# Kernel optimization log

Hardware: AMD Instinct MI355X
Metric: run time of the kernel (lower is better)

The kernel has to match this reference:

```python
import jax, jax.numpy as jnp
import numpy as np

BN, BE, B = 50000, 800000, 16
NE, EE, GE, EH, NH = 32, 32, 32, 128, 128  # emb dims, hidden dims


def clean(x):
    return jnp.nan_to_num(x, nan=0.0, posinf=0.0, neginf=0.0)


def _lin(key, fan_in, fan_out):
    k1, k2 = jax.random.split(key)
    s = 1.0 / np.sqrt(fan_in)
    return (jax.random.uniform(k1, (fan_in, fan_out), jnp.float32, -s, s),
            jax.random.uniform(k2, (fan_out,), jnp.float32, -s, s))


def setup_inputs() -> dict:
    key = jax.random.key(0)
    ks = jax.random.split(key, 20)
    inp = {
        "x": jax.random.normal(ks[0], (BN, 2), jnp.float32),
        "edge_index": jax.random.randint(ks[1], (2, BE), 0, BN, jnp.int32),
        "batch": jax.random.randint(ks[2], (BN,), 0, B, jnp.int32),
        "node_attr": jnp.ones((BN, 2), jnp.float32),
        "edge_attr": jax.random.uniform(ks[3], (BE, 2), jnp.float32) + 0.5,  # positive spacings
        "glob_attr": jax.random.uniform(ks[4], (B, 2), jnp.float32),
    }
    # encoders (output 2*emb each, 'Duplicated')
    inp["enc_node_W"], inp["enc_node_b"] = _lin(ks[5], 2, 2 * NE)
    inp["enc_edge_W"], inp["enc_edge_b"] = _lin(ks[6], 2, 2 * EE)
    inp["enc_glob_W"], inp["enc_glob_b"] = _lin(ks[7], 2, 2 * GE)
    inp["enc2_W"], inp["enc2_b"] = _lin(ks[8], 2, 2 * EE)
    # derivative MLP: 4*NE+2*EE -> EH -> 2*EE
    inp["dW1"], inp["db1"] = _lin(ks[9], 4 * NE + 2 * EE, EH)
    inp["dW2"], inp["db2"] = _lin(ks[10], EH, 2 * EE)
    # half-jacobian MLP: 4*EE -> EH -> 2*EE
    inp["hW1"], inp["hb1"] = _lin(ks[11], 4 * EE, EH)
    inp["hW2"], inp["hb2"] = _lin(ks[12], EH, 2 * EE)
    # jacobian MLP: 6*EE -> NH -> 2*NE
    inp["jW1"], inp["jb1"] = _lin(ks[13], 6 * EE, NH)
    inp["jW2"], inp["jb2"] = _lin(ks[14], NH, 2 * NE)
    # hessian MLP: 4*EE+2*EE -> NH -> 2*NE
    inp["sW1"], inp["sb1"] = _lin(ks[15], 6 * EE, NH)
    inp["sW2"], inp["sb2"] = _lin(ks[16], NH, 2 * NE)
    # node MLP: 6*NE+2*GE -> NH -> 2*NE
    inp["nW1"], inp["nb1"] = _lin(ks[17], 6 * NE + 2 * GE, NH)
    inp["nW2"], inp["nb2"] = _lin(ks[18], NH, 2 * NE)
    # decoder: 2*NE -> 2
    inp["decW"], inp["decb"] = _lin(ks[19], 2 * NE, 2)
    return inp


def reference(x, edge_index, batch, node_attr, edge_attr, glob_attr,
              enc_node_W, enc_node_b, enc_edge_W, enc_edge_b, enc_glob_W, enc_glob_b,
              enc2_W, enc2_b,
              dW1, db1, dW2, db2,
              hW1, hb1, hW2, hb2,
              jW1, jb1, jW2, jb2,
              sW1, sb1, sW2, sb2,
              nW1, nb1, nW2, nb2,
              decW, decb):
    relu = jax.nn.relu
    seg = lambda d, idx: jax.ops.segment_sum(d, idx, num_segments=BN)
    mlp = lambda t, W1, b1, W2, b2: relu(t @ W1 + b1) @ W2 + b2

    row, col = edge_index[0], edge_index[1]
    spacing = edge_attr                                 # [BE,2]
    inv_spacing = clean(1.0 / spacing)
    inv_double = clean(1.0 / (seg(spacing, row) + seg(spacing, col)))  # [BN,2]

    node_emb = relu(x @ enc_node_W + enc_node_b)        # [BN,2*NE]
    spacing_emb = relu(spacing @ enc_edge_W + enc_edge_b)  # [BE,2*EE]
    glob_emb = relu(glob_attr @ enc_glob_W + enc_glob_b)   # [B,2*GE]
    inv_spacing_emb = relu(inv_spacing @ enc2_W + enc2_b)  # [BE,2*EE]
    inv_double_emb = relu(inv_double @ enc2_W + enc2_b)    # [BN,2*EE]

    d_edge = mlp(jnp.concatenate([node_emb[row], node_emb[col], inv_spacing_emb], -1),
                 dW1, db1, dW2, db2)                    # [BE,2*EE]
    hj_plus = seg(d_edge, row)                          # [BN,2*EE]
    hj_minus = seg(d_edge, col)

    jac1 = seg(mlp(jnp.concatenate([spacing_emb, hj_plus[col]], -1), hW1, hb1, hW2, hb2), col)
    jac2 = seg(mlp(jnp.concatenate([spacing_emb, hj_minus[row]], -1), hW1, hb1, hW2, hb2), row)
    jac = mlp(jnp.concatenate([jac1, jac2, inv_double_emb], -1), jW1, jb1, jW2, jb2)  # [BN,2*NE]

    hess = mlp(jnp.concatenate([hj_plus, hj_minus, inv_double_emb], -1), sW1, sb1, sW2, sb2)

    res = mlp(jnp.concatenate([node_emb, jac, glob_emb[batch], hess], -1), nW1, nb1, nW2, nb2)
    return node_attr * (res @ decW + decb)              # [BN,2]
```

## Files before the change

kernel.cpp:

```cpp
#include <hip/hip_runtime.h>
#include <math.h>

#define BN 50000
#define BE 800000

__device__ __forceinline__ float relu_f(float v) { return fmaxf(v, 0.0f); }
__device__ __forceinline__ float inv_clean(float s) {
    float q = 1.0f / s;
    return isfinite(q) ? q : 0.0f;
}
__device__ __forceinline__ float inv_clean_fast(float s) {
    float q = __builtin_amdgcn_rcpf(s);
    return isfinite(q) ? q : 0.0f;
}

__global__ __launch_bounds__(256) void k_node_enc(
    const float* __restrict__ x, const float* __restrict__ W,
    const float* __restrict__ b, float* __restrict__ node_emb)
{
    int t = blockIdx.x * 256 + threadIdx.x;
    int i = t >> 6, l = t & 63;
    float v = fmaf(x[i*2], W[l], fmaf(x[i*2+1], W[64+l], b[l]));
    node_emb[t] = relu_f(v);
}


__global__ __launch_bounds__(256, 2) void k_uv(
    const float* __restrict__ ne, const float* __restrict__ dW1,
    float* __restrict__ u, float* __restrict__ v)
{
    extern __shared__ float lds[];
    float4* wpk = (float4*)lds;
    float*  xbase = lds + 16384;

    for (int idx = threadIdx.x; idx < 64*64; idx += 256) {
        int j = idx >> 6, l = idx & 63;
        float4 w;
        if (l < 32) w = ((const float4*)(dW1 + j*128))[l];
        else        w = ((const float4*)(dW1 + (64+j)*128))[l-32];
        wpk[idx] = w;
    }
    __syncthreads();

    const int wid = threadIdx.x >> 6, l = threadIdx.x & 63;
    float* xb = xbase + wid * 512;
    float4* xb4 = (float4*)xb;
    const int gw = blockIdx.x * 4 + wid;
    const int nw = gridDim.x * 4;

    for (int g = gw; g < BN/8; g += nw) {
        const int n0 = g * 8;
        const int q = l >> 5;
        #pragma unroll
        for (int r = 0; r < 2; r++) {
            int j = (l & 31) + 32*r;
            float v0 = ne[(n0 + q*4 + 0)*64 + j];
            float v1 = ne[(n0 + q*4 + 1)*64 + j];
            float v2 = ne[(n0 + q*4 + 2)*64 + j];
            float v3 = ne[(n0 + q*4 + 3)*64 + j];
            xb4[j*2 + q] = make_float4(v0, v1, v2, v3);
        }
        float4 acc[8];
        #pragma unroll
        for (int e = 0; e < 8; e++) acc[e] = make_float4(0,0,0,0);
        #pragma unroll 8
        for (int j = 0; j < 64; j++) {
            float4 wq = wpk[j*64 + l];
            float4 xa = xb4[j*2 + 0];
            float4 xc = xb4[j*2 + 1];
            acc[0].x = fmaf(xa.x, wq.x, acc[0].x); acc[0].y = fmaf(xa.x, wq.y, acc[0].y);
            acc[0].z = fmaf(xa.x, wq.z, acc[0].z); acc[0].w = fmaf(xa.x, wq.w, acc[0].w);
            acc[1].x = fmaf(xa.y, wq.x, acc[1].x); acc[1].y = fmaf(xa.y, wq.y, acc[1].y);
            acc[1].z = fmaf(xa.y, wq.z, acc[1].z); acc[1].w = fmaf(xa.y, wq.w, acc[1].w);
            acc[2].x = fmaf(xa.z, wq.x, acc[2].x); acc[2].y = fmaf(xa.z, wq.y, acc[2].y);
            acc[2].z = fmaf(xa.z, wq.z, acc[2].z); acc[2].w = fmaf(xa.z, wq.w, acc[2].w);
            acc[3].x = fmaf(xa.w, wq.x, acc[3].x); acc[3].y = fmaf(xa.w, wq.y, acc[3].y);
            acc[3].z = fmaf(xa.w, wq.z, acc[3].z); acc[3].w = fmaf(xa.w, wq.w, acc[3].w);
            acc[4].x = fmaf(xc.x, wq.x, acc[4].x); acc[4].y = fmaf(xc.x, wq.y, acc[4].y);
            acc[4].z = fmaf(xc.x, wq.z, acc[4].z); acc[4].w = fmaf(xc.x, wq.w, acc[4].w);
            acc[5].x = fmaf(xc.y, wq.x, acc[5].x); acc[5].y = fmaf(xc.y, wq.y, acc[5].y);
            acc[5].z = fmaf(xc.y, wq.z, acc[5].z); acc[5].w = fmaf(xc.y, wq.w, acc[5].w);
            acc[6].x = fmaf(xc.z, wq.x, acc[6].x); acc[6].y = fmaf(xc.z, wq.y, acc[6].y);
            acc[6].z = fmaf(xc.z, wq.z, acc[6].z); acc[6].w = fmaf(xc.z, wq.w, acc[6].w);
            acc[7].x = fmaf(xc.w, wq.x, acc[7].x); acc[7].y = fmaf(xc.w, wq.y, acc[7].y);
            acc[7].z = fmaf(xc.w, wq.z, acc[7].z); acc[7].w = fmaf(xc.w, wq.w, acc[7].w);
        }
        float* dst = (l < 32) ? (u + 4*l) : (v + 4*(l-32));
        #pragma unroll
        for (int e = 0; e < 8; e++) {
            *(float4*)(dst + (size_t)(n0+e)*128) = acc[e];
        }
    }
}

__global__ __launch_bounds__(256, 2) void k_tptm(
    const float* __restrict__ hjp, const float* __restrict__ hjm,
    const float* __restrict__ hW1,
    float* __restrict__ tp, float* __restrict__ tm)
{
    extern __shared__ float lds[];
    float4* wpk = (float4*)lds;
    float*  xbase = lds + 8192;

    for (int idx = threadIdx.x; idx < 32*64; idx += 256) {
        int j2 = idx >> 6, l = idx & 63;
        float2 lo = ((const float2*)(hW1 + (64 + 2*j2)*128))[l];
        float2 hi = ((const float2*)(hW1 + (64 + 2*j2 + 1)*128))[l];
        wpk[idx] = make_float4(lo.x, lo.y, hi.x, hi.y);
    }
    __syncthreads();

    const int wid = threadIdx.x >> 6, l = threadIdx.x & 63;
    float* xb = xbase + wid * 512;
    float4* xb4 = (float4*)xb;
    const int gw = blockIdx.x * 4 + wid;
    const int nw = gridDim.x * 4;
    const int NG = BN/8;

    for (int vg = gw; vg < 2*NG; vg += nw) {
        const float* in  = (vg < NG) ? hjp : hjm;
        float*       out = (vg < NG) ? tp  : tm;
        const int n0 = ((vg < NG) ? vg : vg - NG) * 8;
        const int q = l >> 5;
        #pragma unroll
        for (int r = 0; r < 2; r++) {
            int j = (l & 31) + 32*r;
            float v0 = in[(n0 + q*4 + 0)*64 + j];
            float v1 = in[(n0 + q*4 + 1)*64 + j];
            float v2 = in[(n0 + q*4 + 2)*64 + j];
            float v3 = in[(n0 + q*4 + 3)*64 + j];
            xb4[j*2 + q] = make_float4(v0, v1, v2, v3);
        }
        float a0[8] = {0,0,0,0,0,0,0,0}, a1[8] = {0,0,0,0,0,0,0,0};
        #pragma unroll 8
        for (int j2 = 0; j2 < 32; j2++) {
            float4 wq = wpk[j2*64 + l];
            float4 xa = xb4[(2*j2)*2 + 0];
            float4 xbv = xb4[(2*j2)*2 + 1];
            float4 xc = xb4[(2*j2+1)*2 + 0];
            float4 xd = xb4[(2*j2+1)*2 + 1];
            a0[0] = fmaf(xa.x, wq.x, fmaf(xc.x, wq.z, a0[0]));
            a1[0] = fmaf(xa.x, wq.y, fmaf(xc.x, wq.w, a1[0]));
            a0[1] = fmaf(xa.y, wq.x, fmaf(xc.y, wq.z, a0[1]));
            a1[1] = fmaf(xa.y, wq.y, fmaf(xc.y, wq.w, a1[1]));
            a0[2] = fmaf(xa.z, wq.x, fmaf(xc.z, wq.z, a0[2]));
            a1[2] = fmaf(xa.z, wq.y, fmaf(xc.z, wq.w, a1[2]));
            a0[3] = fmaf(xa.w, wq.x, fmaf(xc.w, wq.z, a0[3]));
            a1[3] = fmaf(xa.w, wq.y, fmaf(xc.w, wq.w, a1[3]));
            a0[4] = fmaf(xbv.x, wq.x, fmaf(xd.x, wq.z, a0[4]));
            a1[4] = fmaf(xbv.x, wq.y, fmaf(xd.x, wq.w, a1[4]));
            a0[5] = fmaf(xbv.y, wq.x, fmaf(xd.y, wq.z, a0[5]));
            a1[5] = fmaf(xbv.y, wq.y, fmaf(xd.y, wq.w, a1[5]));
            a0[6] = fmaf(xbv.z, wq.x, fmaf(xd.z, wq.z, a0[6]));
            a1[6] = fmaf(xbv.z, wq.y, fmaf(xd.z, wq.w, a1[6]));
            a0[7] = fmaf(xbv.w, wq.x, fmaf(xd.w, wq.z, a0[7]));
            a1[7] = fmaf(xbv.w, wq.y, fmaf(xd.w, wq.w, a1[7]));
        }
        #pragma unroll
        for (int e = 0; e < 8; e++) {
            *(float2*)(out + (size_t)(n0+e)*128 + 2*l) = make_float2(a0[e], a1[e]);
        }
    }
}

__global__ __launch_bounds__(256, 2) void k_edge1f(
    const int* __restrict__ ei, const float* __restrict__ ea,
    const float* __restrict__ u, const float* __restrict__ v,
    const float* __restrict__ e2w, const float* __restrict__ e2b,
    const float* __restrict__ dW1, const float* __restrict__ db1,
    const float* __restrict__ dW2, const float* __restrict__ db2,
    float* __restrict__ sumsp, float* __restrict__ hjp, float* __restrict__ hjm)
{
    extern __shared__ float lds[];
    float4* w1pk = (float4*)lds;
    float4* w2pk = (float4*)(lds + 8192);
    float*  bufbase = lds + 16384;

    for (int idx = threadIdx.x; idx < 32*64; idx += 256) {
        int j2 = idx >> 6, ll = idx & 63;
        float2 lo = ((const float2*)(dW1 + (128 + 2*j2)*128))[ll];
        float2 hi = ((const float2*)(dW1 + (128 + 2*j2 + 1)*128))[ll];
        w1pk[idx] = make_float4(lo.x, lo.y, hi.x, hi.y);
    }
    for (int idx = threadIdx.x; idx < 32*64; idx += 256) {
        int k4 = idx >> 6, ll = idx & 63;
        w2pk[idx] = make_float4(dW2[(4*k4+0)*64+ll], dW2[(4*k4+1)*64+ll],
                                dW2[(4*k4+2)*64+ll], dW2[(4*k4+3)*64+ll]);
    }
    __syncthreads();

    const int wid = threadIdx.x >> 6, l = threadIdx.x & 63;
    float* buf = bufbase + wid * 1024;
    float4* buf4 = (float4*)buf;

    const int jA = l >> 1;
    const int eh = l & 1;
    const float ewA0 = e2w[jA],      ewB0 = e2w[64+jA],    eb0v = e2b[jA];
    const float ewA1 = e2w[jA+32],   ewB1 = e2w[96+jA],    eb1v = e2b[jA+32];
    const float b1a = db1[2*l], b1b = db1[2*l+1];
    const float b2r = db2[l];

    const int gw = blockIdx.x * 4 + wid;
    const int nw = gridDim.x * 4;

    for (int g = gw; g < BE/8; g += nw) {
        const int e0 = g * 8;
        int4 r01 = *(const int4*)(ei + e0);
        int4 r2  = *(const int4*)(ei + e0 + 4);
        int4 c01 = *(const int4*)(ei + BE + e0);
        int4 c2  = *(const int4*)(ei + BE + e0 + 4);
        float4 sv0 = ((const float4*)(ea + 2*e0))[0];
        float4 sv1 = ((const float4*)(ea + 2*e0))[1];
        float4 sv2 = ((const float4*)(ea + 2*e0))[2];
        float4 sv3 = ((const float4*)(ea + 2*e0))[3];

        if (l < 32) {
            int e = l >> 2, wch = l & 3;
            int4 rA = (e & 4) ? r2 : r01;
            int rx = (e & 2) ? ((e & 1) ? rA.w : rA.z) : ((e & 1) ? rA.y : rA.x);
            int4 cA = (e & 4) ? c2 : c01;
            int cx = (e & 2) ? ((e & 1) ? cA.w : cA.z) : ((e & 1) ? cA.y : cA.x);
            float4 sA = (e & 4) ? ((e & 2) ? sv3 : sv2) : ((e & 2) ? sv1 : sv0);
            float s0e = (e & 1) ? sA.z : sA.x;
            float s1e = (e & 1) ? sA.w : sA.y;
            int node = (wch < 2) ? rx : cx;
            int comp = wch & 1;
            float val = comp ? s1e : s0e;
            atomicAdd(&sumsp[node*2 + comp], val);
        }

        {
            float4 svA = eh ? sv2 : sv0;
            float4 svB = eh ? sv3 : sv1;
            float q00 = inv_clean_fast(svA.x), q10 = inv_clean_fast(svA.y);
            float q01 = inv_clean_fast(svA.z), q11 = inv_clean_fast(svA.w);
            float q02 = inv_clean_fast(svB.x), q12 = inv_clean_fast(svB.y);
            float q03 = inv_clean_fast(svB.z), q13 = inv_clean_fast(svB.w);
            float4 p0, p1;
            p0.x = relu_f(fmaf(q00, ewA0, fmaf(q10, ewB0, eb0v)));
            p0.y = relu_f(fmaf(q01, ewA0, fmaf(q11, ewB0, eb0v)));
            p0.z = relu_f(fmaf(q02, ewA0, fmaf(q12, ewB0, eb0v)));
            p0.w = relu_f(fmaf(q03, ewA0, fmaf(q13, ewB0, eb0v)));
            p1.x = relu_f(fmaf(q00, ewA1, fmaf(q10, ewB1, eb1v)));
            p1.y = relu_f(fmaf(q01, ewA1, fmaf(q11, ewB1, eb1v)));
            p1.z = relu_f(fmaf(q02, ewA1, fmaf(q12, ewB1, eb1v)));
            p1.w = relu_f(fmaf(q03, ewA1, fmaf(q13, ewB1, eb1v)));
            buf4[jA*2 + eh]      = p0;
            buf4[(jA+32)*2 + eh] = p1;
        }

        float t0[8], t1[8];
        {
            const int rr[8] = {r01.x, r01.y, r01.z, r01.w, r2.x, r2.y, r2.z, r2.w};
            const int cc[8] = {c01.x, c01.y, c01.z, c01.w, c2.x, c2.y, c2.z, c2.w};
            #pragma unroll
            for (int e = 0; e < 8; e++) {
                float2 uu = *(const float2*)(u + (size_t)rr[e]*128 + 2*l);
                float2 vv = *(const float2*)(v + (size_t)cc[e]*128 + 2*l);
                t0[e] = b1a + uu.x + vv.x;
                t1[e] = b1b + uu.y + vv.y;
            }
        }

        #pragma unroll 8
        for (int j2 = 0; j2 < 32; j2++) {
            float4 wq = w1pk[j2*64 + l];
            float4 xa = buf4[(2*j2)*2 + 0];
            float4 xbv = buf4[(2*j2)*2 + 1];
            float4 xc = buf4[(2*j2+1)*2 + 0];
            float4 xd = buf4[(2*j2+1)*2 + 1];
            t0[0] = fmaf(xa.x, wq.x, fmaf(xc.x, wq.z, t0[0]));
            t1[0] = fmaf(xa.x, wq.y, fmaf(xc.x, wq.w, t1[0]));
            t0[1] = fmaf(xa.y, wq.x, fmaf(xc.y, wq.z, t0[1]));
            t1[1] = fmaf(xa.y, wq.y, fmaf(xc.y, wq.w, t1[1]));
            t0[2] = fmaf(xa.z, wq.x, fmaf(xc.z, wq.z, t0[2]));
            t1[2] = fmaf(xa.z, wq.y, fmaf(xc.z, wq.w, t1[2]));
            t0[3] = fmaf(xa.w, wq.x, fmaf(xc.w, wq.z, t0[3]));
            t1[3] = fmaf(xa.w, wq.y, fmaf(xc.w, wq.w, t1[3]));
            t0[4] = fmaf(xbv.x, wq.x, fmaf(xd.x, wq.z, t0[4]));
            t1[4] = fmaf(xbv.x, wq.y, fmaf(xd.x, wq.w, t1[4]));
            t0[5] = fmaf(xbv.y, wq.x, fmaf(xd.y, wq.z, t0[5]));
            t1[5] = fmaf(xbv.y, wq.y, fmaf(xd.y, wq.w, t1[5]));
            t0[6] = fmaf(xbv.z, wq.x, fmaf(xd.z, wq.z, t0[6]));
            t1[6] = fmaf(xbv.z, wq.y, fmaf(xd.z, wq.w, t1[6]));
            t0[7] = fmaf(xbv.w, wq.x, fmaf(xd.w, wq.z, t0[7]));
            t1[7] = fmaf(xbv.w, wq.y, fmaf(xd.w, wq.w, t1[7]));
        }

        #pragma unroll
        for (int e = 0; e < 8; e++) {
            *(float2*)(buf + e*128 + 2*l) = make_float2(relu_f(t0[e]), relu_f(t1[e]));
        }
        float o[8] = {0,0,0,0,0,0,0,0};
        #pragma unroll 8
        for (int k4 = 0; k4 < 32; k4++) {
            float4 wq = w2pk[k4*64 + l];
            #pragma unroll
            for (int e = 0; e < 8; e++) {
                float4 hb = *(const float4*)(buf + e*128 + 4*k4);
                o[e] = fmaf(hb.x, wq.x, fmaf(hb.y, wq.y,
                        fmaf(hb.z, wq.z, fmaf(hb.w, wq.w, o[e]))));
            }
        }
        {
            const int rr[8] = {r01.x, r01.y, r01.z, r01.w, r2.x, r2.y, r2.z, r2.w};
            const int cc[8] = {c01.x, c01.y, c01.z, c01.w, c2.x, c2.y, c2.z, c2.w};
            #pragma unroll
            for (int e = 0; e < 8; e++) {
                float ov = o[e] + b2r;
                atomicAdd(&hjp[(size_t)rr[e]*64 + l], ov);
                atomicAdd(&hjm[(size_t)cc[e]*64 + l], ov);
            }
        }
    }
}

__global__ __launch_bounds__(256, 2) void k_edge2f(
    const int* __restrict__ ei, const float* __restrict__ ea,
    const float* __restrict__ tp, const float* __restrict__ tm,
    const float* __restrict__ eew, const float* __restrict__ eeb,
    const float* __restrict__ hW1, const float* __restrict__ hb1,
    const float* __restrict__ hW2, const float* __restrict__ hb2,
    float* __restrict__ jac1, float* __restrict__ jac2)
{
    extern __shared__ float lds[];
    float4* w1pk = (float4*)lds;
    float4* w2pk = (float4*)(lds + 8192);
    float*  bufbase = lds + 16384;

    for (int idx = threadIdx.x; idx < 32*64; idx += 256) {
        int j2 = idx >> 6, ll = idx & 63;
        float2 lo = ((const float2*)(hW1 + (2*j2)*128))[ll];
        float2 hi = ((const float2*)(hW1 + (2*j2 + 1)*128))[ll];
        w1pk[idx] = make_float4(lo.x, lo.y, hi.x, hi.y);
    }
    for (int idx = threadIdx.x; idx < 32*64; idx += 256) {
        int k4 = idx >> 6, ll = idx & 63;
        w2pk[idx] = make_float4(hW2[(4*k4+0)*64+ll], hW2[(4*k4+1)*64+ll],
                                hW2[(4*k4+2)*64+ll], hW2[(4*k4+3)*64+ll]);
    }
    __syncthreads();

    const int wid = threadIdx.x >> 6, l = threadIdx.x & 63;
    float* buf = bufbase + wid * 1024;
    float4* buf4 = (float4*)buf;

    const int jA = l >> 1;
    const int eh = l & 1;
    const float ewA0 = eew[jA],    ewB0 = eew[64+jA],  eb0v = eeb[jA];
    const float ewA1 = eew[jA+32], ewB1 = eew[96+jA],  eb1v = eeb[jA+32];
    const float b1a = hb1[2*l], b1b = hb1[2*l+1];
    const float b2r = hb2[l];

    const int gw = blockIdx.x * 4 + wid;
    const int nw = gridDim.x * 4;

    for (int g = gw; g < BE/8; g += nw) {
        const int e0 = g * 8;
        int4 r01 = *(const int4*)(ei + e0);
        int4 r2  = *(const int4*)(ei + e0 + 4);
        int4 c01 = *(const int4*)(ei + BE + e0);
        int4 c2  = *(const int4*)(ei + BE + e0 + 4);
        float4 sv0 = ((const float4*)(ea + 2*e0))[0];
        float4 sv1 = ((const float4*)(ea + 2*e0))[1];
        float4 sv2 = ((const float4*)(ea + 2*e0))[2];
        float4 sv3 = ((const float4*)(ea + 2*e0))[3];

        {
            float4 svA = eh ? sv2 : sv0;
            float4 svB = eh ? sv3 : sv1;
            float4 p0, p1;
            p0.x = relu_f(fmaf(svA.x, ewA0, fmaf(svA.y, ewB0, eb0v)));
            p0.y = relu_f(fmaf(svA.z, ewA0, fmaf(svA.w, ewB0, eb0v)));
            p0.z = relu_f(fmaf(svB.x, ewA0, fmaf(svB.y, ewB0, eb0v)));
            p0.w = relu_f(fmaf(svB.z, ewA0, fmaf(svB.w, ewB0, eb0v)));
            p1.x = relu_f(fmaf(svA.x, ewA1, fmaf(svA.y, ewB1, eb1v)));
            p1.y = relu_f(fmaf(svA.z, ewA1, fmaf(svA.w, ewB1, eb1v)));
            p1.z = relu_f(fmaf(svB.x, ewA1, fmaf(svB.y, ewB1, eb1v)));
            p1.w = relu_f(fmaf(svB.z, ewA1, fmaf(svB.w, ewB1, eb1v)));
            buf4[jA*2 + eh]      = p0;
            buf4[(jA+32)*2 + eh] = p1;
        }

        const int rr[8] = {r01.x, r01.y, r01.z, r01.w, r2.x, r2.y, r2.z, r2.w};
        const int cc[8] = {c01.x, c01.y, c01.z, c01.w, c2.x, c2.y, c2.z, c2.w};

        float2 tpv[8];
        #pragma unroll
        for (int e = 0; e < 8; e++)
            tpv[e] = *(const float2*)(tp + (size_t)cc[e]*128 + 2*l);

        float t0[8], t1[8];
        #pragma unroll
        for (int e = 0; e < 8; e++) { t0[e] = b1a; t1[e] = b1b; }

        #pragma unroll 8
        for (int j2 = 0; j2 < 32; j2++) {
            float4 wq = w1pk[j2*64 + l];
            float4 xa = buf4[(2*j2)*2 + 0];
            float4 xbv = buf4[(2*j2)*2 + 1];
            float4 xc = buf4[(2*j2+1)*2 + 0];
            float4 xd = buf4[(2*j2+1)*2 + 1];
            t0[0] = fmaf(xa.x, wq.x, fmaf(xc.x, wq.z, t0[0]));
            t1[0] = fmaf(xa.x, wq.y, fmaf(xc.x, wq.w, t1[0]));
            t0[1] = fmaf(xa.y, wq.x, fmaf(xc.y, wq.z, t0[1]));
            t1[1] = fmaf(xa.y, wq.y, fmaf(xc.y, wq.w, t1[1]));
            t0[2] = fmaf(xa.z, wq.x, fmaf(xc.z, wq.z, t0[2]));
            t1[2] = fmaf(xa.z, wq.y, fmaf(xc.z, wq.w, t1[2]));
            t0[3] = fmaf(xa.w, wq.x, fmaf(xc.w, wq.z, t0[3]));
            t1[3] = fmaf(xa.w, wq.y, fmaf(xc.w, wq.w, t1[3]));
            t0[4] = fmaf(xbv.x, wq.x, fmaf(xd.x, wq.z, t0[4]));
            t1[4] = fmaf(xbv.x, wq.y, fmaf(xd.x, wq.w, t1[4]));
            t0[5] = fmaf(xbv.y, wq.x, fmaf(xd.y, wq.z, t0[5]));
            t1[5] = fmaf(xbv.y, wq.y, fmaf(xd.y, wq.w, t1[5]));
            t0[6] = fmaf(xbv.z, wq.x, fmaf(xd.z, wq.z, t0[6]));
            t1[6] = fmaf(xbv.z, wq.y, fmaf(xd.z, wq.w, t1[6]));
            t0[7] = fmaf(xbv.w, wq.x, fmaf(xd.w, wq.z, t0[7]));
            t1[7] = fmaf(xbv.w, wq.y, fmaf(xd.w, wq.w, t1[7]));
        }

        #pragma unroll
        for (int e = 0; e < 8; e++) {
            *(float2*)(buf + e*128 + 2*l) =
                make_float2(relu_f(t0[e] + tpv[e].x), relu_f(t1[e] + tpv[e].y));
        }
        float2 tmv[8];
        #pragma unroll
        for (int e = 0; e < 8; e++)
            tmv[e] = *(const float2*)(tm + (size_t)rr[e]*128 + 2*l);

        float o1[8] = {0,0,0,0,0,0,0,0};
        #pragma unroll 8
        for (int k4 = 0; k4 < 32; k4++) {
            float4 wq = w2pk[k4*64 + l];
            #pragma unroll
            for (int e = 0; e < 8; e++) {
                float4 hb = *(const float4*)(buf + e*128 + 4*k4);
                o1[e] = fmaf(hb.x, wq.x, fmaf(hb.y, wq.y,
                         fmaf(hb.z, wq.z, fmaf(hb.w, wq.w, o1[e]))));
            }
        }
        #pragma unroll
        for (int e = 0; e < 8; e++)
            atomicAdd(&jac1[(size_t)cc[e]*64 + l], o1[e] + b2r);

        #pragma unroll
        for (int e = 0; e < 8; e++) {
            *(float2*)(buf + e*128 + 2*l) =
                make_float2(relu_f(t0[e] + tmv[e].x), relu_f(t1[e] + tmv[e].y));
        }
        float o2[8] = {0,0,0,0,0,0,0,0};
        #pragma unroll 8
        for (int k4 = 0; k4 < 32; k4++) {
            float4 wq = w2pk[k4*64 + l];
            #pragma unroll
            for (int e = 0; e < 8; e++) {
                float4 hb = *(const float4*)(buf + e*128 + 4*k4);
                o2[e] = fmaf(hb.x, wq.x, fmaf(hb.y, wq.y,
                         fmaf(hb.z, wq.z, fmaf(hb.w, wq.w, o2[e]))));
            }
        }
        #pragma unroll
        for (int e = 0; e < 8; e++)
            atomicAdd(&jac2[(size_t)rr[e]*64 + l], o2[e] + b2r);
    }
}

__global__ __launch_bounds__(256) void k_edge1(
    const int* __restrict__ ei, const float* __restrict__ ea,
    const float* __restrict__ node_emb,
    const float* __restrict__ e2w_g, const float* __restrict__ e2b_g,
    const float* __restrict__ dW1, const float* __restrict__ db1,
    const float* __restrict__ dW2, const float* __restrict__ db2,
    float* __restrict__ sumsp, float* __restrict__ hjp, float* __restrict__ hjm)
{
    extern __shared__ float lds[];
    float* w1 = lds;
    float* b1 = w1 + 192*128;
    float* w2 = b1 + 128;
    float* b2 = w2 + 128*64;
    float* ew = b2 + 64;
    float* eb = ew + 128;
    float* xreg = eb + 64;
    float* hreg = xreg + 4*768;

    for (int idx = threadIdx.x; idx < 192*128; idx += 256) w1[idx] = dW1[idx];
    for (int idx = threadIdx.x; idx < 128*64; idx += 256)  w2[idx] = dW2[idx];
    if (threadIdx.x < 128) { b1[threadIdx.x] = db1[threadIdx.x]; ew[threadIdx.x] = e2w_g[threadIdx.x]; }
    if (threadIdx.x < 64)  { b2[threadIdx.x] = db2[threadIdx.x]; eb[threadIdx.x] = e2b_g[threadIdx.x]; }
    __syncthreads();

    const int wid = threadIdx.x >> 6, l = threadIdx.x & 63;
    float* xbuf = xreg + wid * 768;
    float* hbuf = hreg + wid * 512;
    const int gw = blockIdx.x * 4 + wid;
    const int nw = gridDim.x * 4;

    for (int g = gw; g < BE/4; g += nw) {
        const int e0 = g * 4;
        int r[4], c[4];
        float s0[4], s1[4];
        #pragma unroll
        for (int e = 0; e < 4; e++) {
            r[e]  = ei[e0+e];
            c[e]  = ei[BE + e0+e];
            s0[e] = ea[(e0+e)*2+0];
            s1[e] = ea[(e0+e)*2+1];
        }
        if (l < 16) {
            int e = l >> 2, wch = l & 3;
            int node = (wch < 2) ? r[e] : c[e];
            float v = (wch & 1) ? s1[e] : s0[e];
            atomicAdd(&sumsp[node*2 + (wch & 1)], v);
        }
        float ar[4], cr[4], ir[4];
        #pragma unroll
        for (int e = 0; e < 4; e++) {
            ar[e] = node_emb[r[e]*64 + l];
            cr[e] = node_emb[c[e]*64 + l];
            float q0 = inv_clean(s0[e]), q1 = inv_clean(s1[e]);
            ir[e] = relu_f(fmaf(q0, ew[l], fmaf(q1, ew[64+l], eb[l])));
        }
        ((float4*)xbuf)[l]       = make_float4(ar[0], ar[1], ar[2], ar[3]);
        ((float4*)xbuf)[64 + l]  = make_float4(cr[0], cr[1], cr[2], cr[3]);
        ((float4*)xbuf)[128 + l] = make_float4(ir[0], ir[1], ir[2], ir[3]);

        float acc0[4] = {0,0,0,0}, acc1[4] = {0,0,0,0};
        #pragma unroll 8
        for (int j = 0; j < 192; j++) {
            float4 xv = ((const float4*)xbuf)[j];
            float2 wv = ((const float2*)(w1 + j*128))[l];
            acc0[0] = fmaf(xv.x, wv.x, acc0[0]);
            acc0[1] = fmaf(xv.y, wv.x, acc0[1]);
            acc0[2] = fmaf(xv.z, wv.x, acc0[2]);
            acc0[3] = fmaf(xv.w, wv.x, acc0[3]);
            acc1[0] = fmaf(xv.x, wv.y, acc1[0]);
            acc1[1] = fmaf(xv.y, wv.y, acc1[1]);
            acc1[2] = fmaf(xv.z, wv.y, acc1[2]);
            acc1[3] = fmaf(xv.w, wv.y, acc1[3]);
        }
        float bb0 = b1[2*l], bb1 = b1[2*l+1];
        #pragma unroll
        for (int e = 0; e < 4; e++) {
            float2 h = make_float2(relu_f(acc0[e]+bb0), relu_f(acc1[e]+bb1));
            ((float2*)(hbuf + e*128))[l] = h;
        }
        float o[4] = {0,0,0,0};
        #pragma unroll 8
        for (int k = 0; k < 128; k++) {
            float wv = w2[k*64 + l];
            o[0] = fmaf(hbuf[0*128+k], wv, o[0]);
            o[1] = fmaf(hbuf[1*128+k], wv, o[1]);
            o[2] = fmaf(hbuf[2*128+k], wv, o[2]);
            o[3] = fmaf(hbuf[3*128+k], wv, o[3]);
        }
        float bo = b2[l];
        #pragma unroll
        for (int e = 0; e < 4; e++) {
            float ov = o[e] + bo;
            atomicAdd(&hjp[r[e]*64 + l], ov);
            atomicAdd(&hjm[c[e]*64 + l], ov);
        }
    }
}

__global__ __launch_bounds__(256) void k_edge2(
    const int* __restrict__ ei, const float* __restrict__ ea,
    const float* __restrict__ hjp, const float* __restrict__ hjm,
    const float* __restrict__ eew_g, const float* __restrict__ eeb_g,
    const float* __restrict__ hW1, const float* __restrict__ hb1,
    const float* __restrict__ hW2, const float* __restrict__ hb2,
    float* __restrict__ jac1, float* __restrict__ jac2)
{
    extern __shared__ float lds[];
    float* w1 = lds;
    float* b1 = w1 + 128*128;
    float* w2 = b1 + 128;
    float* b2 = w2 + 128*64;
    float* ew = b2 + 64;
    float* eb = ew + 128;
    float* base = eb + 64;

    for (int idx = threadIdx.x; idx < 128*128; idx += 256) w1[idx] = hW1[idx];
    for (int idx = threadIdx.x; idx < 128*64; idx += 256)  w2[idx] = hW2[idx];
    if (threadIdx.x < 128) { b1[threadIdx.x] = hb1[threadIdx.x]; ew[threadIdx.x] = eew_g[threadIdx.x]; }
    if (threadIdx.x < 64)  { b2[threadIdx.x] = hb2[threadIdx.x]; eb[threadIdx.x] = eeb_g[threadIdx.x]; }
    __syncthreads();

    const int wid = threadIdx.x >> 6, l = threadIdx.x & 63;
    float* x1 = base + wid*2048;
    float* x2 = x1 + 512;
    float* h1 = x2 + 512;
    float* h2 = h1 + 512;
    const int gw = blockIdx.x * 4 + wid;
    const int nw = gridDim.x * 4;

    for (int g = gw; g < BE/4; g += nw) {
        const int e0 = g * 4;
        int r[4], c[4];
        float se[4], pa[4], pb[4];
        #pragma unroll
        for (int e = 0; e < 4; e++) {
            r[e] = ei[e0+e];
            c[e] = ei[BE + e0+e];
            float sp0 = ea[(e0+e)*2+0], sp1 = ea[(e0+e)*2+1];
            se[e] = relu_f(fmaf(sp0, ew[l], fmaf(sp1, ew[64+l], eb[l])));
            pa[e] = hjp[c[e]*64 + l];
            pb[e] = hjm[r[e]*64 + l];
        }
        ((float4*)x1)[l]      = make_float4(se[0], se[1], se[2], se[3]);
        ((float4*)x1)[64 + l] = make_float4(pa[0], pa[1], pa[2], pa[3]);
        ((float4*)x2)[l]      = make_float4(se[0], se[1], se[2], se[3]);
        ((float4*)x2)[64 + l] = make_float4(pb[0], pb[1], pb[2], pb[3]);

        float a0[4]={0,0,0,0}, a1[4]={0,0,0,0}, b0v[4]={0,0,0,0}, b1v[4]={0,0,0,0};
        #pragma unroll 8
        for (int j = 0; j < 128; j++) {
            float2 wv = ((const float2*)(w1 + j*128))[l];
            float4 xa = ((const float4*)x1)[j];
            float4 xb = ((const float4*)x2)[j];
            a0[0]=fmaf(xa.x,wv.x,a0[0]); a0[1]=fmaf(xa.y,wv.x,a0[1]);
            a0[2]=fmaf(xa.z,wv.x,a0[2]); a0[3]=fmaf(xa.w,wv.x,a0[3]);
            a1[0]=fmaf(xa.x,wv.y,a1[0]); a1[1]=fmaf(xa.y,wv.y,a1[1]);
            a1[2]=fmaf(xa.z,wv.y,a1[2]); a1[3]=fmaf(xa.w,wv.y,a1[3]);
            b0v[0]=fmaf(xb.x,wv.x,b0v[0]); b0v[1]=fmaf(xb.y,wv.x,b0v[1]);
            b0v[2]=fmaf(xb.z,wv.x,b0v[2]); b0v[3]=fmaf(xb.w,wv.x,b0v[3]);
            b1v[0]=fmaf(xb.x,wv.y,b1v[0]); b1v[1]=fmaf(xb.y,wv.y,b1v[1]);
            b1v[2]=fmaf(xb.z,wv.y,b1v[2]); b1v[3]=fmaf(xb.w,wv.y,b1v[3]);
        }
        float bb0 = b1[2*l], bb1 = b1[2*l+1];
        #pragma unroll
        for (int e = 0; e < 4; e++) {
            ((float2*)(h1 + e*128))[l] = make_float2(relu_f(a0[e]+bb0), relu_f(a1[e]+bb1));
            ((float2*)(h2 + e*128))[l] = make_float2(relu_f(b0v[e]+bb0), relu_f(b1v[e]+bb1));
        }
        float oA[4]={0,0,0,0}, oB[4]={0,0,0,0};
        #pragma unroll 8
        for (int k = 0; k < 128; k++) {
            float wv = w2[k*64 + l];
            oA[0]=fmaf(h1[0*128+k],wv,oA[0]); oA[1]=fmaf(h1[1*128+k],wv,oA[1]);
            oA[2]=fmaf(h1[2*128+k],wv,oA[2]); oA[3]=fmaf(h1[3*128+k],wv,oA[3]);
            oB[0]=fmaf(h2[0*128+k],wv,oB[0]); oB[1]=fmaf(h2[1*128+k],wv,oB[1]);
            oB[2]=fmaf(h2[2*128+k],wv,oB[2]); oB[3]=fmaf(h2[3*128+k],wv,oB[3]);
        }
        float bo = b2[l];
        #pragma unroll
        for (int e = 0; e < 4; e++) {
            atomicAdd(&jac1[c[e]*64 + l], oA[e] + bo);
            atomicAdd(&jac2[r[e]*64 + l], oB[e] + bo);
        }
    }
}

__global__ __launch_bounds__(256) void k_node_mlp(
    const float* __restrict__ A, const float* __restrict__ Bv,
    const float* __restrict__ sumsp,
    const float* __restrict__ e2w_g, const float* __restrict__ e2b_g,
    const float* __restrict__ W1g, const float* __restrict__ b1g,
    const float* __restrict__ W2g, const float* __restrict__ b2g,
    float* __restrict__ outp)
{
    extern __shared__ float lds[];
    float* w1 = lds;
    float* b1 = w1 + 192*128;
    float* w2 = b1 + 128;
    float* b2 = w2 + 128*64;
    float* ew = b2 + 64;
    float* eb = ew + 128;
    float* xreg = eb + 64;
    float* hreg = xreg + 4*768;

    for (int idx = threadIdx.x; idx < 192*128; idx += 256) w1[idx] = W1g[idx];
    for (int idx = threadIdx.x; idx < 128*64; idx += 256)  w2[idx] = W2g[idx];
    if (threadIdx.x < 128) { b1[threadIdx.x] = b1g[threadIdx.x]; ew[threadIdx.x] = e2w_g[threadIdx.x]; }
    if (threadIdx.x < 64)  { b2[threadIdx.x] = b2g[threadIdx.x]; eb[threadIdx.x] = e2b_g[threadIdx.x]; }
    __syncthreads();

    const int wid = threadIdx.x >> 6, l = threadIdx.x & 63;
    float* xbuf = xreg + wid * 768;
    float* hbuf = hreg + wid * 512;
    const int gw = blockIdx.x * 4 + wid;
    const int nw = gridDim.x * 4;

    for (int g = gw; g < BN/4; g += nw) {
        const int i0 = g * 4;
        float av[4], bv[4], iv[4];
        #pragma unroll
        for (int e = 0; e < 4; e++) {
            int i = i0 + e;
            av[e] = A[i*64 + l];
            bv[e] = Bv[i*64 + l];
            float q0 = inv_clean(sumsp[i*2+0]);
            float q1 = inv_clean(sumsp[i*2+1]);
            iv[e] = relu_f(fmaf(q0, ew[l], fmaf(q1, ew[64+l], eb[l])));
        }
        ((float4*)xbuf)[l]       = make_float4(av[0], av[1], av[2], av[3]);
        ((float4*)xbuf)[64 + l]  = make_float4(bv[0], bv[1], bv[2], bv[3]);
        ((float4*)xbuf)[128 + l] = make_float4(iv[0], iv[1], iv[2], iv[3]);

        float acc0[4] = {0,0,0,0}, acc1[4] = {0,0,0,0};
        #pragma unroll 8
        for (int j = 0; j < 192; j++) {
            float4 xv = ((const float4*)xbuf)[j];
            float2 wv = ((const float2*)(w1 + j*128))[l];
            acc0[0] = fmaf(xv.x, wv.x, acc0[0]);
            acc0[1] = fmaf(xv.y, wv.x, acc0[1]);
            acc0[2] = fmaf(xv.z, wv.x, acc0[2]);
            acc0[3] = fmaf(xv.w, wv.x, acc0[3]);
            acc1[0] = fmaf(xv.x, wv.y, acc1[0]);
            acc1[1] = fmaf(xv.y, wv.y, acc1[1]);
            acc1[2] = fmaf(xv.z, wv.y, acc1[2]);
            acc1[3] = fmaf(xv.w, wv.y, acc1[3]);
        }
        float bb0 = b1[2*l], bb1 = b1[2*l+1];
        #pragma unroll
        for (int e = 0; e < 4; e++) {
            ((float2*)(hbuf + e*128))[l] = make_float2(relu_f(acc0[e]+bb0), relu_f(acc1[e]+bb1));
        }
        float o[4] = {0,0,0,0};
        #pragma unroll 8
        for (int k = 0; k < 128; k++) {
            float wv = w2[k*64 + l];
            o[0] = fmaf(hbuf[0*128+k], wv, o[0]);
            o[1] = fmaf(hbuf[1*128+k], wv, o[1]);
            o[2] = fmaf(hbuf[2*128+k], wv, o[2]);
            o[3] = fmaf(hbuf[3*128+k], wv, o[3]);
        }
        float bo = b2[l];
        #pragma unroll
        for (int e = 0; e < 4; e++) outp[(i0+e)*64 + l] = o[e] + bo;
    }
}

__global__ __launch_bounds__(256) void k_node_final(
    const float* __restrict__ node_emb, const float* __restrict__ jacv,
    const float* __restrict__ hessv,
    const int* __restrict__ batch, const float* __restrict__ ga,
    const float* __restrict__ gw_g, const float* __restrict__ gb_g,
    const float* __restrict__ nW1, const float* __restrict__ nb1,
    const float* __restrict__ nW2, const float* __restrict__ nb2,
    const float* __restrict__ decW, const float* __restrict__ decb,
    const float* __restrict__ node_attr, float* __restrict__ outp)
{
    extern __shared__ float lds[];
    float* w1 = lds;
    float* b1 = w1 + 256*128;
    float* b2 = b1 + 128;
    float* gw = b2 + 64;
    float* gb = gw + 128;
    float* dw = gb + 64;
    float* db = dw + 128;
    float* xreg = db + 4;
    float* hreg = xreg + 4*1024;

    for (int idx = threadIdx.x; idx < 256*128; idx += 256) w1[idx] = nW1[idx];
    if (threadIdx.x < 128) { b1[threadIdx.x] = nb1[threadIdx.x]; gw[threadIdx.x] = gw_g[threadIdx.x]; dw[threadIdx.x] = decW[threadIdx.x]; }
    if (threadIdx.x < 64)  { b2[threadIdx.x] = nb2[threadIdx.x]; gb[threadIdx.x] = gb_g[threadIdx.x]; }
    if (threadIdx.x < 2)   { db[threadIdx.x] = decb[threadIdx.x]; }
    __syncthreads();

    const int wid = threadIdx.x >> 6, l = threadIdx.x & 63;
    float* xbuf = xreg + wid * 1024;
    float* hbuf = hreg + wid * 512;
    const int gwv = blockIdx.x * 4 + wid;
    const int nw = gridDim.x * 4;

    for (int g = gwv; g < BN/4; g += nw) {
        const int i0 = g * 4;
        float ne[4], jv[4], ge[4], hv[4];
        #pragma unroll
        for (int e = 0; e < 4; e++) {
            int i = i0 + e;
            ne[e] = node_emb[i*64 + l];
            jv[e] = jacv[i*64 + l];
            hv[e] = hessv[i*64 + l];
            int gi = batch[i];
            ge[e] = relu_f(fmaf(ga[gi*2], gw[l], fmaf(ga[gi*2+1], gw[64+l], gb[l])));
        }
        ((float4*)xbuf)[l]       = make_float4(ne[0], ne[1], ne[2], ne[3]);
        ((float4*)xbuf)[64 + l]  = make_float4(jv[0], jv[1], jv[2], jv[3]);
        ((float4*)xbuf)[128 + l] = make_float4(ge[0], ge[1], ge[2], ge[3]);
        ((float4*)xbuf)[192 + l] = make_float4(hv[0], hv[1], hv[2], hv[3]);

        float acc0[4] = {0,0,0,0}, acc1[4] = {0,0,0,0};
        #pragma unroll 8
        for (int j = 0; j < 256; j++) {
            float4 xv = ((const float4*)xbuf)[j];
            float2 wv = ((const float2*)(w1 + j*128))[l];
            acc0[0] = fmaf(xv.x, wv.x, acc0[0]);
            acc0[1] = fmaf(xv.y, wv.x, acc0[1]);
            acc0[2] = fmaf(xv.z, wv.x, acc0[2]);
            acc0[3] = fmaf(xv.w, wv.x, acc0[3]);
            acc1[0] = fmaf(xv.x, wv.y, acc1[0]);
            acc1[1] = fmaf(xv.y, wv.y, acc1[1]);
            acc1[2] = fmaf(xv.z, wv.y, acc1[2]);
            acc1[3] = fmaf(xv.w, wv.y, acc1[3]);
        }
        float bb0 = b1[2*l], bb1 = b1[2*l+1];
        #pragma unroll
        for (int e = 0; e < 4; e++) {
            ((float2*)(hbuf + e*128))[l] = make_float2(relu_f(acc0[e]+bb0), relu_f(acc1[e]+bb1));
        }
        float o[4] = {0,0,0,0};
        #pragma unroll 8
        for (int k = 0; k < 128; k++) {
            float wv = nW2[k*64 + l];
            o[0] = fmaf(hbuf[0*128+k], wv, o[0]);
            o[1] = fmaf(hbuf[1*128+k], wv, o[1]);
            o[2] = fmaf(hbuf[2*128+k], wv, o[2]);
            o[3] = fmaf(hbuf[3*128+k], wv, o[3]);
        }
        float bo = b2[l];
        #pragma unroll
        for (int e = 0; e < 4; e++) hbuf[e*128 + l] = o[e] + bo;

        int e2 = l >> 4, sub = l & 15, j2 = sub >> 3, part = sub & 7;
        float s = 0.0f;
        #pragma unroll
        for (int kk = 0; kk < 8; kk++) {
            int k = part*8 + kk;
            s = fmaf(hbuf[e2*128 + k], dw[k*2 + j2], s);
        }
        s += __shfl_xor(s, 1);
        s += __shfl_xor(s, 2);
        s += __shfl_xor(s, 4);
        if (part == 0) {
            int i = i0 + e2;
            outp[i*2 + j2] = (s + db[j2]) * node_attr[i*2 + j2];
        }
    }
}

extern "C" void kernel_launch(void* const* d_in, const int* in_sizes, int n_in,
                              void* d_out, int out_size, void* d_ws, size_t ws_size,
                              hipStream_t stream) {
    const float* x          = (const float*)d_in[0];
    const int*   ei         = (const int*)  d_in[1];
    const int*   batch      = (const int*)  d_in[2];
    const float* node_attr  = (const float*)d_in[3];
    const float* edge_attr  = (const float*)d_in[4];
    const float* glob_attr  = (const float*)d_in[5];
    const float* enc_node_W = (const float*)d_in[6];
    const float* enc_node_b = (const float*)d_in[7];
    const float* enc_edge_W = (const float*)d_in[8];
    const float* enc_edge_b = (const float*)d_in[9];
    const float* enc_glob_W = (const float*)d_in[10];
    const float* enc_glob_b = (const float*)d_in[11];
    const float* enc2_W     = (const float*)d_in[12];
    const float* enc2_b     = (const float*)d_in[13];
    const float* dW1 = (const float*)d_in[14]; const float* db1 = (const float*)d_in[15];
    const float* dW2 = (const float*)d_in[16]; const float* db2 = (const float*)d_in[17];
    const float* hW1 = (const float*)d_in[18]; const float* hb1 = (const float*)d_in[19];
    const float* hW2 = (const float*)d_in[20]; const float* hb2 = (const float*)d_in[21];
    const float* jW1 = (const float*)d_in[22]; const float* jb1 = (const float*)d_in[23];
    const float* jW2 = (const float*)d_in[24]; const float* jb2 = (const float*)d_in[25];
    const float* sW1 = (const float*)d_in[26]; const float* sb1 = (const float*)d_in[27];
    const float* sW2 = (const float*)d_in[28]; const float* sb2 = (const float*)d_in[29];
    const float* nW1 = (const float*)d_in[30]; const float* nb1 = (const float*)d_in[31];
    const float* nW2 = (const float*)d_in[32]; const float* nb2 = (const float*)d_in[33];
    const float* decW = (const float*)d_in[34]; const float* decb = (const float*)d_in[35];

    float* ws = (float*)d_ws;
    const size_t NEED_FAST = 28900000ull * sizeof(float);

    if (ws_size >= NEED_FAST) {
        float* ne    = ws;
        float* u     = ne + 3200000;
        float* v     = u + 6400000;
        float* hjp   = v + 6400000;
        float* hjm   = hjp + 3200000;
        float* jac1  = hjm + 3200000;
        float* jac2  = jac1 + 3200000;
        float* sumsp = jac2 + 3200000;

        hipMemsetAsync(hjp, 0, (size_t)4*3200000*sizeof(float), stream);
        hipMemsetAsync(sumsp, 0, (size_t)100000*sizeof(float), stream);

        k_node_enc<<<12500, 256, 0, stream>>>(x, enc_node_W, enc_node_b, ne);

        size_t lds_uv = 18432u * sizeof(float);
        k_uv<<<512, 256, lds_uv, stream>>>(ne, dW1, u, v);

        size_t lds_e = 20480u * sizeof(float);
        k_edge1f<<<512, 256, lds_e, stream>>>(ei, edge_attr, u, v, enc2_W, enc2_b,
                                              dW1, db1, dW2, db2, sumsp, hjp, hjm);

        size_t lds_tptm = 10240u * sizeof(float);
        k_tptm<<<512, 256, lds_tptm, stream>>>(hjp, hjm, hW1, u, v);

        k_edge2f<<<512, 256, lds_e, stream>>>(ei, edge_attr, u, v,
                                              enc_edge_W, enc_edge_b,
                                              hW1, hb1, hW2, hb2, jac1, jac2);

        size_t lds3 = 38272u * sizeof(float);
        k_node_mlp<<<256, 256, lds3, stream>>>(jac1, jac2, sumsp, enc2_W, enc2_b,
                                               jW1, jb1, jW2, jb2, jac1);
        k_node_mlp<<<256, 256, lds3, stream>>>(hjp, hjm, sumsp, enc2_W, enc2_b,
                                               sW1, sb1, sW2, sb2, hjp);

        size_t lds4 = 39428u * sizeof(float);
        k_node_final<<<256, 256, lds4, stream>>>(ne, jac1, hjp,
                                                 batch, glob_attr, enc_glob_W, enc_glob_b,
                                                 nW1, nb1, nW2, nb2, decW, decb,
                                                 node_attr, (float*)d_out);
    } else {
        float* node_emb = ws;
        float* hjp   = node_emb + 3200000;
        float* hjm   = hjp + 3200000;
        float* jac1  = hjm + 3200000;
        float* jac2  = jac1 + 3200000;
        float* sumsp = jac2 + 3200000;

        hipMemsetAsync(hjp, 0, (size_t)4*3200000*sizeof(float), stream);
        hipMemsetAsync(sumsp, 0, (size_t)100000*sizeof(float), stream);

        k_node_enc<<<12500, 256, 0, stream>>>(x, enc_node_W, enc_node_b, node_emb);

        size_t lds1 = 38272u * sizeof(float);
        k_edge1<<<256, 256, lds1, stream>>>(ei, edge_attr, node_emb, enc2_W, enc2_b,
                                            dW1, db1, dW2, db2, sumsp, hjp, hjm);

        size_t lds2 = 33152u * sizeof(float);
        k_edge2<<<256, 256, lds2, stream>>>(ei, edge_attr, hjp, hjm,
                                            enc_edge_W, enc_edge_b,
                                            hW1, hb1, hW2, hb2, jac1, jac2);

        size_t lds3 = 38272u * sizeof(float);
        k_node_mlp<<<256, 256, lds3, stream>>>(jac1, jac2, sumsp, enc2_W, enc2_b,
                                               jW1, jb1, jW2, jb2, jac1);
        k_node_mlp<<<256, 256, lds3, stream>>>(hjp, hjm, sumsp, enc2_W, enc2_b,
                                               sW1, sb1, sW2, sb2, hjp);

        size_t lds4 = 39428u * sizeof(float);
        k_node_final<<<256, 256, lds4, stream>>>(node_emb, jac1, hjp,
                                                 batch, glob_attr, enc_glob_W, enc_glob_b,
                                                 nW1, nb1, nW2, nb2, decW, decb,
                                                 node_attr, (float*)d_out);
    }
}
```

Measured before the change: 2.139 ms.

## Move MLP weights from LDS to pre-packed global memory to raise occupancy

Weight matrices that every block used to stage into LDS are now packed once into global scratch by small pack kernels, or read straight from global in the node kernels. The main kernels are served through the cache instead. With LDS use cut to per-wave activation buffers, launch bounds rise to 6 (4 for node kernels) and grids grow to 1536/1024 blocks to improve latency hiding. The trade-off is that weight loads now go through the L1/L2 cache rather than LDS. The packed weights are stored in the output buffer as scratch before the final kernel overwrites it.

```diff
diff --git a/kernel.cpp b/kernel.cpp
--- a/kernel.cpp
+++ b/kernel.cpp
@@ -14,6 +14,37 @@
     return isfinite(q) ? q : 0.0f;
 }
 
+__global__ __launch_bounds__(256) void k_pack_w1(
+    const float* __restrict__ W, int r0, float4* __restrict__ dst)
+{
+    int t = blockIdx.x * 256 + threadIdx.x;
+    if (t >= 2048) return;
+    int j2 = t >> 6, l = t & 63;
+    const float* ra = W + (size_t)(r0 + 2*j2) * 128 + 2*l;
+    const float* rb = W + (size_t)(r0 + 2*j2 + 1) * 128 + 2*l;
+    dst[t] = make_float4(ra[0], ra[1], rb[0], rb[1]);
+}
+__global__ __launch_bounds__(256) void k_pack_w2(
+    const float* __restrict__ W2, float4* __restrict__ dst)
+{
+    int t = blockIdx.x * 256 + threadIdx.x;
+    if (t >= 2048) return;
+    int k4 = t >> 6, l = t & 63;
+    dst[t] = make_float4(W2[(4*k4+0)*64+l], W2[(4*k4+1)*64+l],
+                         W2[(4*k4+2)*64+l], W2[(4*k4+3)*64+l]);
+}
+__global__ __launch_bounds__(256) void k_pack_uv(
+    const float* __restrict__ dW1, float4* __restrict__ dst)
+{
+    int t = blockIdx.x * 256 + threadIdx.x;
+    if (t >= 4096) return;
+    int j = t >> 6, l = t & 63;
+    float4 w;
+    if (l < 32) w = ((const float4*)(dW1 + (size_t)j*128))[l];
+    else        w = ((const float4*)(dW1 + (size_t)(64+j)*128))[l-32];
+    dst[t] = w;
+}
+
 __global__ __launch_bounds__(256) void k_node_enc(
     const float* __restrict__ x, const float* __restrict__ W,
     const float* __restrict__ b, float* __restrict__ node_emb)
@@ -25,26 +56,13 @@
 }
 
 
-__global__ __launch_bounds__(256, 2) void k_uv(
-    const float* __restrict__ ne, const float* __restrict__ dW1,
+__global__ __launch_bounds__(256, 6) void k_uv(
+    const float* __restrict__ ne, const float4* __restrict__ guv,
     float* __restrict__ u, float* __restrict__ v)
 {
     extern __shared__ float lds[];
-    float4* wpk = (float4*)lds;
-    float*  xbase = lds + 16384;
-
-    for (int idx = threadIdx.x; idx < 64*64; idx += 256) {
-        int j = idx >> 6, l = idx & 63;
-        float4 w;
-        if (l < 32) w = ((const float4*)(dW1 + j*128))[l];
-        else        w = ((const float4*)(dW1 + (64+j)*128))[l-32];
-        wpk[idx] = w;
-    }
-    __syncthreads();
-
     const int wid = threadIdx.x >> 6, l = threadIdx.x & 63;
-    float* xb = xbase + wid * 512;
-    float4* xb4 = (float4*)xb;
+    float4* xb4 = (float4*)(lds + wid * 512);
     const int gw = blockIdx.x * 4 + wid;
     const int nw = gridDim.x * 4;
 
@@ -65,7 +83,7 @@
         for (int e = 0; e < 8; e++) acc[e] = make_float4(0,0,0,0);
         #pragma unroll 8
         for (int j = 0; j < 64; j++) {
-            float4 wq = wpk[j*64 + l];
+            float4 wq = guv[j*64 + l];
             float4 xa = xb4[j*2 + 0];
             float4 xc = xb4[j*2 + 1];
             acc[0].x = fmaf(xa.x, wq.x, acc[0].x); acc[0].y = fmaf(xa.x, wq.y, acc[0].y);
@@ -93,26 +111,14 @@
     }
 }
 
-__global__ __launch_bounds__(256, 2) void k_tptm(
+__global__ __launch_bounds__(256, 6) void k_tptm(
     const float* __restrict__ hjp, const float* __restrict__ hjm,
-    const float* __restrict__ hW1,
+    const float4* __restrict__ gtp,
     float* __restrict__ tp, float* __restrict__ tm)
 {
     extern __shared__ float lds[];
-    float4* wpk = (float4*)lds;
-    float*  xbase = lds + 8192;
-
-    for (int idx = threadIdx.x; idx < 32*64; idx += 256) {
-        int j2 = idx >> 6, l = idx & 63;
-        float2 lo = ((const float2*)(hW1 + (64 + 2*j2)*128))[l];
-        float2 hi = ((const float2*)(hW1 + (64 + 2*j2 + 1)*128))[l];
-        wpk[idx] = make_float4(lo.x, lo.y, hi.x, hi.y);
-    }
-    __syncthreads();
-
     const int wid = threadIdx.x >> 6, l = threadIdx.x & 63;
-    float* xb = xbase + wid * 512;
-    float4* xb4 = (float4*)xb;
+    float4* xb4 = (float4*)(lds + wid * 512);
     const int gw = blockIdx.x * 4 + wid;
     const int nw = gridDim.x * 4;
     const int NG = BN/8;
@@ -134,7 +140,7 @@
         float a0[8] = {0,0,0,0,0,0,0,0}, a1[8] = {0,0,0,0,0,0,0,0};
         #pragma unroll 8
         for (int j2 = 0; j2 < 32; j2++) {
-            float4 wq = wpk[j2*64 + l];
+            float4 wq = gtp[j2*64 + l];
             float4 xa = xb4[(2*j2)*2 + 0];
             float4 xbv = xb4[(2*j2)*2 + 1];
             float4 xc = xb4[(2*j2+1)*2 + 0];
@@ -163,34 +169,17 @@
     }
 }
 
-__global__ __launch_bounds__(256, 2) void k_edge1f(
+__global__ __launch_bounds__(256, 6) void k_edge1f(
     const int* __restrict__ ei, const float* __restrict__ ea,
     const float* __restrict__ u, const float* __restrict__ v,
     const float* __restrict__ e2w, const float* __restrict__ e2b,
-    const float* __restrict__ dW1, const float* __restrict__ db1,
-    const float* __restrict__ dW2, const float* __restrict__ db2,
+    const float4* __restrict__ gw1, const float* __restrict__ db1,
+    const float4* __restrict__ gw2, const float* __restrict__ db2,
     float* __restrict__ sumsp, float* __restrict__ hjp, float* __restrict__ hjm)
 {
     extern __shared__ float lds[];
-    float4* w1pk = (float4*)lds;
-    float4* w2pk = (float4*)(lds + 8192);
-    float*  bufbase = lds + 16384;
-
-    for (int idx = threadIdx.x; idx < 32*64; idx += 256) {
-        int j2 = idx >> 6, ll = idx & 63;
-        float2 lo = ((const float2*)(dW1 + (128 + 2*j2)*128))[ll];
-        float2 hi = ((const float2*)(dW1 + (128 + 2*j2 + 1)*128))[ll];
-        w1pk[idx] = make_float4(lo.x, lo.y, hi.x, hi.y);
-    }
-    for (int idx = threadIdx.x; idx < 32*64; idx += 256) {
-        int k4 = idx >> 6, ll = idx & 63;
-        w2pk[idx] = make_float4(dW2[(4*k4+0)*64+ll], dW2[(4*k4+1)*64+ll],
-                                dW2[(4*k4+2)*64+ll], dW2[(4*k4+3)*64+ll]);
-    }
-    __syncthreads();
-
     const int wid = threadIdx.x >> 6, l = threadIdx.x & 63;
-    float* buf = bufbase + wid * 1024;
+    float* buf = lds + wid * 1024;
     float4* buf4 = (float4*)buf;
 
     const int jA = l >> 1;
@@ -264,7 +253,7 @@
 
         #pragma unroll 8
         for (int j2 = 0; j2 < 32; j2++) {
-            float4 wq = w1pk[j2*64 + l];
+            float4 wq = gw1[j2*64 + l];
             float4 xa = buf4[(2*j2)*2 + 0];
             float4 xbv = buf4[(2*j2)*2 + 1];
             float4 xc = buf4[(2*j2+1)*2 + 0];
@@ -294,7 +283,7 @@
         float o[8] = {0,0,0,0,0,0,0,0};
         #pragma unroll 8
         for (int k4 = 0; k4 < 32; k4++) {
-            float4 wq = w2pk[k4*64 + l];
+            float4 wq = gw2[k4*64 + l];
             #pragma unroll
             for (int e = 0; e < 8; e++) {
                 float4 hb = *(const float4*)(buf + e*128 + 4*k4);
@@ -315,34 +304,17 @@
     }
 }
 
-__global__ __launch_bounds__(256, 2) void k_edge2f(
+__global__ __launch_bounds__(256, 6) void k_edge2f(
     const int* __restrict__ ei, const float* __restrict__ ea,
     const float* __restrict__ tp, const float* __restrict__ tm,
     const float* __restrict__ eew, const float* __restrict__ eeb,
-    const float* __restrict__ hW1, const float* __restrict__ hb1,
-    const float* __restrict__ hW2, const float* __restrict__ hb2,
+    const float4* __restrict__ gw1, const float* __restrict__ hb1,
+    const float4* __restrict__ gw2, const float* __restrict__ hb2,
     float* __restrict__ jac1, float* __restrict__ jac2)
 {
     extern __shared__ float lds[];
-    float4* w1pk = (float4*)lds;
-    float4* w2pk = (float4*)(lds + 8192);
-    float*  bufbase = lds + 16384;
-
-    for (int idx = threadIdx.x; idx < 32*64; idx += 256) {
-        int j2 = idx >> 6, ll = idx & 63;
-        float2 lo = ((const float2*)(hW1 + (2*j2)*128))[ll];
-        float2 hi = ((const float2*)(hW1 + (2*j2 + 1)*128))[ll];
-        w1pk[idx] = make_float4(lo.x, lo.y, hi.x, hi.y);
-    }
-    for (int idx = threadIdx.x; idx < 32*64; idx += 256) {
-        int k4 = idx >> 6, ll = idx & 63;
-        w2pk[idx] = make_float4(hW2[(4*k4+0)*64+ll], hW2[(4*k4+1)*64+ll],
-                                hW2[(4*k4+2)*64+ll], hW2[(4*k4+3)*64+ll]);
-    }
-    __syncthreads();
-
     const int wid = threadIdx.x >> 6, l = threadIdx.x & 63;
-    float* buf = bufbase + wid * 1024;
+    float* buf = lds + wid * 1024;
     float4* buf4 = (float4*)buf;
 
     const int jA = l >> 1;
@@ -396,7 +368,7 @@
 
         #pragma unroll 8
         for (int j2 = 0; j2 < 32; j2++) {
-            float4 wq = w1pk[j2*64 + l];
+            float4 wq = gw1[j2*64 + l];
             float4 xa = buf4[(2*j2)*2 + 0];
             float4 xbv = buf4[(2*j2)*2 + 1];
             float4 xc = buf4[(2*j2+1)*2 + 0];
@@ -432,7 +404,7 @@
         float o1[8] = {0,0,0,0,0,0,0,0};
         #pragma unroll 8
         for (int k4 = 0; k4 < 32; k4++) {
-            float4 wq = w2pk[k4*64 + l];
+            float4 wq = gw2[k4*64 + l];
             #pragma unroll
             for (int e = 0; e < 8; e++) {
                 float4 hb = *(const float4*)(buf + e*128 + 4*k4);
@@ -452,7 +424,7 @@
         float o2[8] = {0,0,0,0,0,0,0,0};
         #pragma unroll 8
         for (int k4 = 0; k4 < 32; k4++) {
-            float4 wq = w2pk[k4*64 + l];
+            float4 wq = gw2[k4*64 + l];
             #pragma unroll
             for (int e = 0; e < 8; e++) {
                 float4 hb = *(const float4*)(buf + e*128 + 4*k4);
@@ -463,6 +435,160 @@
         #pragma unroll
         for (int e = 0; e < 8; e++)
             atomicAdd(&jac2[(size_t)rr[e]*64 + l], o2[e] + b2r);
+    }
+}
+
+__global__ __launch_bounds__(256, 4) void k_node_mlp(
+    const float* __restrict__ A, const float* __restrict__ Bv,
+    const float* __restrict__ sumsp,
+    const float* __restrict__ e2w_g, const float* __restrict__ e2b_g,
+    const float* __restrict__ W1g, const float* __restrict__ b1g,
+    const float* __restrict__ W2g, const float* __restrict__ b2g,
+    float* __restrict__ outp)
+{
+    extern __shared__ float lds[];
+    const int wid = threadIdx.x >> 6, l = threadIdx.x & 63;
+    float* xbuf = lds + wid * 768;
+    float* hbuf = lds + 4*768 + wid * 512;
+
+    const float ewl = e2w_g[l], ewl2 = e2w_g[64+l], ebl = e2b_g[l];
+    const float bb0 = b1g[2*l], bb1 = b1g[2*l+1];
+    const float bo = b2g[l];
+
+    const int gw = blockIdx.x * 4 + wid;
+    const int nw = gridDim.x * 4;
+
+    for (int g = gw; g < BN/4; g += nw) {
+        const int i0 = g * 4;
+        float av[4], bv[4], iv[4];
+        #pragma unroll
+        for (int e = 0; e < 4; e++) {
+            int i = i0 + e;
+            av[e] = A[i*64 + l];
+            bv[e] = Bv[i*64 + l];
+            float q0 = inv_clean(sumsp[i*2+0]);
+            float q1 = inv_clean(sumsp[i*2+1]);
+            iv[e] = relu_f(fmaf(q0, ewl, fmaf(q1, ewl2, ebl)));
+        }
+        ((float4*)xbuf)[l]       = make_float4(av[0], av[1], av[2], av[3]);
+        ((float4*)xbuf)[64 + l]  = make_float4(bv[0], bv[1], bv[2], bv[3]);
+        ((float4*)xbuf)[128 + l] = make_float4(iv[0], iv[1], iv[2], iv[3]);
+
+        float acc0[4] = {0,0,0,0}, acc1[4] = {0,0,0,0};
+        #pragma unroll 8
+        for (int j = 0; j < 192; j++) {
+            float4 xv = ((const float4*)xbuf)[j];
+            float2 wv = ((const float2*)(W1g + j*128))[l];
+            acc0[0] = fmaf(xv.x, wv.x, acc0[0]);
+            acc0[1] = fmaf(xv.y, wv.x, acc0[1]);
+            acc0[2] = fmaf(xv.z, wv.x, acc0[2]);
+            acc0[3] = fmaf(xv.w, wv.x, acc0[3]);
+            acc1[0] = fmaf(xv.x, wv.y, acc1[0]);
+            acc1[1] = fmaf(xv.y, wv.y, acc1[1]);
+            acc1[2] = fmaf(xv.z, wv.y, acc1[2]);
+            acc1[3] = fmaf(xv.w, wv.y, acc1[3]);
+        }
+        #pragma unroll
+        for (int e = 0; e < 4; e++) {
+            ((float2*)(hbuf + e*128))[l] = make_float2(relu_f(acc0[e]+bb0), relu_f(acc1[e]+bb1));
+        }
+        float o[4] = {0,0,0,0};
+        #pragma unroll 8
+        for (int k = 0; k < 128; k++) {
+            float wv = W2g[k*64 + l];
+            o[0] = fmaf(hbuf[0*128+k], wv, o[0]);
+            o[1] = fmaf(hbuf[1*128+k], wv, o[1]);
+            o[2] = fmaf(hbuf[2*128+k], wv, o[2]);
+            o[3] = fmaf(hbuf[3*128+k], wv, o[3]);
+        }
+        #pragma unroll
+        for (int e = 0; e < 4; e++) outp[(i0+e)*64 + l] = o[e] + bo;
+    }
+}
+
+__global__ __launch_bounds__(256, 4) void k_node_final(
+    const float* __restrict__ node_emb, const float* __restrict__ jacv,
+    const float* __restrict__ hessv,
+    const int* __restrict__ batch, const float* __restrict__ ga,
+    const float* __restrict__ gw_g, const float* __restrict__ gb_g,
+    const float* __restrict__ nW1, const float* __restrict__ nb1,
+    const float* __restrict__ nW2, const float* __restrict__ nb2,
+    const float* __restrict__ decW, const float* __restrict__ decb,
+    const float* __restrict__ node_attr, float* __restrict__ outp)
+{
+    extern __shared__ float lds[];
+    const int wid = threadIdx.x >> 6, l = threadIdx.x & 63;
+    float* xbuf = lds + wid * 1024;
+    float* hbuf = lds + 4*1024 + wid * 512;
+
+    const float gwl = gw_g[l], gwl2 = gw_g[64+l], gbl = gb_g[l];
+    const float bb0 = nb1[2*l], bb1 = nb1[2*l+1];
+    const float bo = nb2[l];
+
+    const int gwv = blockIdx.x * 4 + wid;
+    const int nw = gridDim.x * 4;
+
+    for (int g = gwv; g < BN/4; g += nw) {
+        const int i0 = g * 4;
+        float ne[4], jv[4], ge[4], hv[4];
+        #pragma unroll
+        for (int e = 0; e < 4; e++) {
+            int i = i0 + e;
+            ne[e] = node_emb[i*64 + l];
+            jv[e] = jacv[i*64 + l];
+            hv[e] = hessv[i*64 + l];
+            int gi = batch[i];
+            ge[e] = relu_f(fmaf(ga[gi*2], gwl, fmaf(ga[gi*2+1], gwl2, gbl)));
+        }
+        ((float4*)xbuf)[l]       = make_float4(ne[0], ne[1], ne[2], ne[3]);
+        ((float4*)xbuf)[64 + l]  = make_float4(jv[0], jv[1], jv[2], jv[3]);
+        ((float4*)xbuf)[128 + l] = make_float4(ge[0], ge[1], ge[2], ge[3]);
+        ((float4*)xbuf)[192 + l] = make_float4(hv[0], hv[1], hv[2], hv[3]);
+
+        float acc0[4] = {0,0,0,0}, acc1[4] = {0,0,0,0};
+        #pragma unroll 8
+        for (int j = 0; j < 256; j++) {
+            float4 xv = ((const float4*)xbuf)[j];
+            float2 wv = ((const float2*)(nW1 + j*128))[l];
+            acc0[0] = fmaf(xv.x, wv.x, acc0[0]);
+            acc0[1] = fmaf(xv.y, wv.x, acc0[1]);
+            acc0[2] = fmaf(xv.z, wv.x, acc0[2]);
+            acc0[3] = fmaf(xv.w, wv.x, acc0[3]);
+            acc1[0] = fmaf(xv.x, wv.y, acc1[0]);
+            acc1[1] = fmaf(xv.y, wv.y, acc1[1]);
+            acc1[2] = fmaf(xv.z, wv.y, acc1[2]);
+            acc1[3] = fmaf(xv.w, wv.y, acc1[3]);
+        }
+        #pragma unroll
+        for (int e = 0; e < 4; e++) {
+            ((float2*)(hbuf + e*128))[l] = make_float2(relu_f(acc0[e]+bb0), relu_f(acc1[e]+bb1));
+        }
+        float o[4] = {0,0,0,0};
+        #pragma unroll 8
+        for (int k = 0; k < 128; k++) {
+            float wv = nW2[k*64 + l];
+            o[0] = fmaf(hbuf[0*128+k], wv, o[0]);
+            o[1] = fmaf(hbuf[1*128+k], wv, o[1]);
+            o[2] = fmaf(hbuf[2*128+k], wv, o[2]);
+            o[3] = fmaf(hbuf[3*128+k], wv, o[3]);
+        }
+        #pragma unroll
+        for (int e = 0; e < 4; e++) hbuf[e*128 + l] = o[e] + bo;
+
+        int e2 = l >> 4, sub = l & 15, j2 = sub >> 3, part = sub & 7;
+        float s = 0.0f;
+        #pragma unroll
+        for (int kk = 0; kk < 8; kk++) {
+            int k = part*8 + kk;
+            s = fmaf(hbuf[e2*128 + k], decW[k*2 + j2], s);
+        }
+        s += __shfl_xor(s, 1);
+        s += __shfl_xor(s, 2);
+        s += __shfl_xor(s, 4);
+        if (part == 0) {
+            int i = i0 + e2;
+            outp[i*2 + j2] = (s + decb[j2]) * node_attr[i*2 + j2];
+        }
     }
 }
 
@@ -648,185 +774,6 @@
         for (int e = 0; e < 4; e++) {
             atomicAdd(&jac1[c[e]*64 + l], oA[e] + bo);
             atomicAdd(&jac2[r[e]*64 + l], oB[e] + bo);
-        }
-    }
-}
-
-__global__ __launch_bounds__(256) void k_node_mlp(
-    const float* __restrict__ A, const float* __restrict__ Bv,
-    const float* __restrict__ sumsp,
-    const float* __restrict__ e2w_g, const float* __restrict__ e2b_g,
-    const float* __restrict__ W1g, const float* __restrict__ b1g,
-    const float* __restrict__ W2g, const float* __restrict__ b2g,
-    float* __restrict__ outp)
-{
-    extern __shared__ float lds[];
-    float* w1 = lds;
-    float* b1 = w1 + 192*128;
-    float* w2 = b1 + 128;
-    float* b2 = w2 + 128*64;
-    float* ew = b2 + 64;
-    float* eb = ew + 128;
-    float* xreg = eb + 64;
-    float* hreg = xreg + 4*768;
-
-    for (int idx = threadIdx.x; idx < 192*128; idx += 256) w1[idx] = W1g[idx];
-    for (int idx = threadIdx.x; idx < 128*64; idx += 256)  w2[idx] = W2g[idx];
-    if (threadIdx.x < 128) { b1[threadIdx.x] = b1g[threadIdx.x]; ew[threadIdx.x] = e2w_g[threadIdx.x]; }
-    if (threadIdx.x < 64)  { b2[threadIdx.x] = b2g[threadIdx.x]; eb[threadIdx.x] = e2b_g[threadIdx.x]; }
-    __syncthreads();
-
-    const int wid = threadIdx.x >> 6, l = threadIdx.x & 63;
-    float* xbuf = xreg + wid * 768;
-    float* hbuf = hreg + wid * 512;
-    const int gw = blockIdx.x * 4 + wid;
-    const int nw = gridDim.x * 4;
-
-    for (int g = gw; g < BN/4; g += nw) {
-        const int i0 = g * 4;
-        float av[4], bv[4], iv[4];
-        #pragma unroll
-        for (int e = 0; e < 4; e++) {
-            int i = i0 + e;
-            av[e] = A[i*64 + l];
-            bv[e] = Bv[i*64 + l];
-            float q0 = inv_clean(sumsp[i*2+0]);
-            float q1 = inv_clean(sumsp[i*2+1]);
-            iv[e] = relu_f(fmaf(q0, ew[l], fmaf(q1, ew[64+l], eb[l])));
-        }
-        ((float4*)xbuf)[l]       = make_float4(av[0], av[1], av[2], av[3]);
-        ((float4*)xbuf)[64 + l]  = make_float4(bv[0], bv[1], bv[2], bv[3]);
-        ((float4*)xbuf)[128 + l] = make_float4(iv[0], iv[1], iv[2], iv[3]);
-
-        float acc0[4] = {0,0,0,0}, acc1[4] = {0,0,0,0};
-        #pragma unroll 8
-        for (int j = 0; j < 192; j++) {
-            float4 xv = ((const float4*)xbuf)[j];
-            float2 wv = ((const float2*)(w1 + j*128))[l];
-            acc0[0] = fmaf(xv.x, wv.x, acc0[0]);
-            acc0[1] = fmaf(xv.y, wv.x, acc0[1]);
-            acc0[2] = fmaf(xv.z, wv.x, acc0[2]);
-            acc0[3] = fmaf(xv.w, wv.x, acc0[3]);
-            acc1[0] = fmaf(xv.x, wv.y, acc1[0]);
-            acc1[1] = fmaf(xv.y, wv.y, acc1[1]);
-            acc1[2] = fmaf(xv.z, wv.y, acc1[2]);
-            acc1[3] = fmaf(xv.w, wv.y, acc1[3]);
-        }
-        float bb0 = b1[2*l], bb1 = b1[2*l+1];
-        #pragma unroll
-        for (int e = 0; e < 4; e++) {
-            ((float2*)(hbuf + e*128))[l] = make_float2(relu_f(acc0[e]+bb0), relu_f(acc1[e]+bb1));
-        }
-        float o[4] = {0,0,0,0};
-        #pragma unroll 8
-        for (int k = 0; k < 128; k++) {
-            float wv = w2[k*64 + l];
-            o[0] = fmaf(hbuf[0*128+k], wv, o[0]);
-            o[1] = fmaf(hbuf[1*128+k], wv, o[1]);
-            o[2] = fmaf(hbuf[2*128+k], wv, o[2]);
-            o[3] = fmaf(hbuf[3*128+k], wv, o[3]);
-        }
-        float bo = b2[l];
-        #pragma unroll
-        for (int e = 0; e < 4; e++) outp[(i0+e)*64 + l] = o[e] + bo;
-    }
-}
-
-__global__ __launch_bounds__(256) void k_node_final(
-    const float* __restrict__ node_emb, const float* __restrict__ jacv,
-    const float* __restrict__ hessv,
-    const int* __restrict__ batch, const float* __restrict__ ga,
-    const float* __restrict__ gw_g, const float* __restrict__ gb_g,
-    const float* __restrict__ nW1, const float* __restrict__ nb1,
-    const float* __restrict__ nW2, const float* __restrict__ nb2,
-    const float* __restrict__ decW, const float* __restrict__ decb,
-    const float* __restrict__ node_attr, float* __restrict__ outp)
-{
-    extern __shared__ float lds[];
-    float* w1 = lds;
-    float* b1 = w1 + 256*128;
-    float* b2 = b1 + 128;
-    float* gw = b2 + 64;
-    float* gb = gw + 128;
-    float* dw = gb + 64;
-    float* db = dw + 128;
-    float* xreg = db + 4;
-    float* hreg = xreg + 4*1024;
-
-    for (int idx = threadIdx.x; idx < 256*128; idx += 256) w1[idx] = nW1[idx];
-    if (threadIdx.x < 128) { b1[threadIdx.x] = nb1[threadIdx.x]; gw[threadIdx.x] = gw_g[threadIdx.x]; dw[threadIdx.x] = decW[threadIdx.x]; }
-    if (threadIdx.x < 64)  { b2[threadIdx.x] = nb2[threadIdx.x]; gb[threadIdx.x] = gb_g[threadIdx.x]; }
-    if (threadIdx.x < 2)   { db[threadIdx.x] = decb[threadIdx.x]; }
-    __syncthreads();
-
-    const int wid = threadIdx.x >> 6, l = threadIdx.x & 63;
-    float* xbuf = xreg + wid * 1024;
-    float* hbuf = hreg + wid * 512;
-    const int gwv = blockIdx.x * 4 + wid;
-    const int nw = gridDim.x * 4;
-
-    for (int g = gwv; g < BN/4; g += nw) {
-        const int i0 = g * 4;
-        float ne[4], jv[4], ge[4], hv[4];
-        #pragma unroll
-        for (int e = 0; e < 4; e++) {
-            int i = i0 + e;
-            ne[e] = node_emb[i*64 + l];
-            jv[e] = jacv[i*64 + l];
-            hv[e] = hessv[i*64 + l];
-            int gi = batch[i];
-            ge[e] = relu_f(fmaf(ga[gi*2], gw[l], fmaf(ga[gi*2+1], gw[64+l], gb[l])));
-        }
-        ((float4*)xbuf)[l]       = make_float4(ne[0], ne[1], ne[2], ne[3]);
-        ((float4*)xbuf)[64 + l]  = make_float4(jv[0], jv[1], jv[2], jv[3]);
-        ((float4*)xbuf)[128 + l] = make_float4(ge[0], ge[1], ge[2], ge[3]);
-        ((float4*)xbuf)[192 + l] = make_float4(hv[0], hv[1], hv[2], hv[3]);
-
-        float acc0[4] = {0,0,0,0}, acc1[4] = {0,0,0,0};
-        #pragma unroll 8
-        for (int j = 0; j < 256; j++) {
-            float4 xv = ((const float4*)xbuf)[j];
-            float2 wv = ((const float2*)(w1 + j*128))[l];
-            acc0[0] = fmaf(xv.x, wv.x, acc0[0]);
-            acc0[1] = fmaf(xv.y, wv.x, acc0[1]);
-            acc0[2] = fmaf(xv.z, wv.x, acc0[2]);
-            acc0[3] = fmaf(xv.w, wv.x, acc0[3]);
-            acc1[0] = fmaf(xv.x, wv.y, acc1[0]);
-            acc1[1] = fmaf(xv.y, wv.y, acc1[1]);
-            acc1[2] = fmaf(xv.z, wv.y, acc1[2]);
-            acc1[3] = fmaf(xv.w, wv.y, acc1[3]);
-        }
-        float bb0 = b1[2*l], bb1 = b1[2*l+1];
-        #pragma unroll
-        for (int e = 0; e < 4; e++) {
-            ((float2*)(hbuf + e*128))[l] = make_float2(relu_f(acc0[e]+bb0), relu_f(acc1[e]+bb1));
-        }
-        float o[4] = {0,0,0,0};
-        #pragma unroll 8
-        for (int k = 0; k < 128; k++) {
-            float wv = nW2[k*64 + l];
-            o[0] = fmaf(hbuf[0*128+k], wv, o[0]);
-            o[1] = fmaf(hbuf[1*128+k], wv, o[1]);
-            o[2] = fmaf(hbuf[2*128+k], wv, o[2]);
-            o[3] = fmaf(hbuf[3*128+k], wv, o[3]);
-        }
-        float bo = b2[l];
-        #pragma unroll
-        for (int e = 0; e < 4; e++) hbuf[e*128 + l] = o[e] + bo;
-
-        int e2 = l >> 4, sub = l & 15, j2 = sub >> 3, part = sub & 7;
-        float s = 0.0f;
-        #pragma unroll
-        for (int kk = 0; kk < 8; kk++) {
-            int k = part*8 + kk;
-            s = fmaf(hbuf[e2*128 + k], dw[k*2 + j2], s);
-        }
-        s += __shfl_xor(s, 1);
-        s += __shfl_xor(s, 2);
-        s += __shfl_xor(s, 4);
-        if (part == 0) {
-            int i = i0 + e2;
-            outp[i*2 + j2] = (s + db[j2]) * node_attr[i*2 + j2];
         }
     }
 }
@@ -873,36 +820,48 @@
         float* jac2  = jac1 + 3200000;
         float* sumsp = jac2 + 3200000;
 
+        float* scratch = (float*)d_out;
+        float4* puv   = (float4*)(scratch);
+        float4* pw1e1 = (float4*)(scratch + 16384);
+        float4* pw2e1 = (float4*)(scratch + 24576);
+        float4* pw1tp = (float4*)(scratch + 32768);
+        float4* pw1e2 = (float4*)(scratch + 40960);
+        float4* pw2e2 = (float4*)(scratch + 49152);
+
         hipMemsetAsync(hjp, 0, (size_t)4*3200000*sizeof(float), stream);
         hipMemsetAsync(sumsp, 0, (size_t)100000*sizeof(float), stream);
 
+        k_pack_uv<<<16, 256, 0, stream>>>(dW1, puv);
+        k_pack_w1<<<8, 256, 0, stream>>>(dW1, 128, pw1e1);
+        k_pack_w2<<<8, 256, 0, stream>>>(dW2, pw2e1);
+        k_pack_w1<<<8, 256, 0, stream>>>(hW1, 64, pw1tp);
+        k_pack_w1<<<8, 256, 0, stream>>>(hW1, 0, pw1e2);
+        k_pack_w2<<<8, 256, 0, stream>>>(hW2, pw2e2);
+
         k_node_enc<<<12500, 256, 0, stream>>>(x, enc_node_W, enc_node_b, ne);
 
-        size_t lds_uv = 18432u * sizeof(float);
-        k_uv<<<512, 256, lds_uv, stream>>>(ne, dW1, u, v);
-
-        size_t lds_e = 20480u * sizeof(float);
-        k_edge1f<<<512, 256, lds_e, stream>>>(ei, edge_attr, u, v, enc2_W, enc2_b,
-                                              dW1, db1, dW2, db2, sumsp, hjp, hjm);
-
-        size_t lds_tptm = 10240u * sizeof(float);
-        k_tptm<<<512, 256, lds_tptm, stream>>>(hjp, hjm, hW1, u, v);
-
-        k_edge2f<<<512, 256, lds_e, stream>>>(ei, edge_attr, u, v,
-                                              enc_edge_W, enc_edge_b,
-                                              hW1, hb1, hW2, hb2, jac1, jac2);
-
-        size_t lds3 = 38272u * sizeof(float);
-        k_node_mlp<<<256, 256, lds3, stream>>>(jac1, jac2, sumsp, enc2_W, enc2_b,
-                                               jW1, jb1, jW2, jb2, jac1);
-        k_node_mlp<<<256, 256, lds3, stream>>>(hjp, hjm, sumsp, enc2_W, enc2_b,
-                                               sW1, sb1, sW2, sb2, hjp);
-
-        size_t lds4 = 39428u * sizeof(float);
-        k_node_final<<<256, 256, lds4, stream>>>(ne, jac1, hjp,
-                                                 batch, glob_attr, enc_glob_W, enc_glob_b,
-                                                 nW1, nb1, nW2, nb2, decW, decb,
-                                                 node_attr, (float*)d_out);
+        k_uv<<<1536, 256, 2048*4, stream>>>(ne, puv, u, v);
+
+        k_edge1f<<<1536, 256, 4096*4, stream>>>(ei, edge_attr, u, v, enc2_W, enc2_b,
+                                                pw1e1, db1, pw2e1, db2, sumsp, hjp, hjm);
+
+        k_tptm<<<1536, 256, 2048*4, stream>>>(hjp, hjm, pw1tp, u, v);
+
+        k_edge2f<<<1536, 256, 4096*4, stream>>>(ei, edge_attr, u, v,
+                                                enc_edge_W, enc_edge_b,
+                                                pw1e2, hb1, pw2e2, hb2, jac1, jac2);
+
+        size_t lds_nm = (4*768 + 4*512) * sizeof(float);
+        k_node_mlp<<<1024, 256, lds_nm, stream>>>(jac1, jac2, sumsp, enc2_W, enc2_b,
+                                                  jW1, jb1, jW2, jb2, jac1);
+        k_node_mlp<<<1024, 256, lds_nm, stream>>>(hjp, hjm, sumsp, enc2_W, enc2_b,
+                                                  sW1, sb1, sW2, sb2, hjp);
+
+        size_t lds_nf = (4*1024 + 4*512) * sizeof(float);
+        k_node_final<<<1024, 256, lds_nf, stream>>>(ne, jac1, hjp,
+                                                    batch, glob_attr, enc_glob_W, enc_glob_b,
+                                                    nW1, nb1, nW2, nb2, decW, decb,
+                                                    node_attr, (float*)d_out);
     } else {
         float* node_emb = ws;
         float* hjp   = node_emb + 3200000;
@@ -925,16 +884,16 @@
                                             enc_edge_W, enc_edge_b,
                                             hW1, hb1, hW2, hb2, jac1, jac2);
 
-        size_t lds3 = 38272u * sizeof(float);
-        k_node_mlp<<<256, 256, lds3, stream>>>(jac1, jac2, sumsp, enc2_W, enc2_b,
-                                               jW1, jb1, jW2, jb2, jac1);
-        k_node_mlp<<<256, 256, lds3, stream>>>(hjp, hjm, sumsp, enc2_W, enc2_b,
-                                               sW1, sb1, sW2, sb2, hjp);
-
-        size_t lds4 = 39428u * sizeof(float);
-        k_node_final<<<256, 256, lds4, stream>>>(node_emb, jac1, hjp,
-                                                 batch, glob_attr, enc_glob_W, enc_glob_b,
-                                                 nW1, nb1, nW2, nb2, decW, decb,
-                                                 node_attr, (float*)d_out);
+        size_t lds_nm = (4*768 + 4*512) * sizeof(float);
+        k_node_mlp<<<1024, 256, lds_nm, stream>>>(jac1, jac2, sumsp, enc2_W, enc2_b,
+                                                  jW1, jb1, jW2, jb2, jac1);
+        k_node_mlp<<<1024, 256, lds_nm, stream>>>(hjp, hjm, sumsp, enc2_W, enc2_b,
+                                                  sW1, sb1, sW2, sb2, hjp);
+
+        size_t lds_nf = (4*1024 + 4*512) * sizeof(float);
+        k_node_final<<<1024, 256, lds_nf, stream>>>(node_emb, jac1, hjp,
+                                                    batch, glob_attr, enc_glob_W, enc_glob_b,
+                                                    nW1, nb1, nW2, nb2, decW, decb,
+                                                    node_attr, (float*)d_out);
     }
 }
```

Result: faster. 2.092 ms (-2.2%).
